# Optimization experiments

Hardware: AMD Instinct MI355X
Metric: run time of the kernel (lower is better)

## Reference

```python
import jax, jax.numpy as jnp
import numpy as np
from jax import lax

K = 5      # reassembly kernel
D = 2      # delta (downsample factor)


def _conv(x, w, b, stride=1, pad=0):
    y = lax.conv_general_dilated(x, w, (stride, stride), [(pad, pad), (pad, pad)],
                                 dimension_numbers=("NCHW", "OIHW", "NCHW"))
    return y + b[None, :, None, None]


def setup_inputs() -> dict:
    key = jax.random.key(0)
    ks = jax.random.split(key, 7)
    inC, outC, Cm = 64, 64, 64
    N, H, W = 2, 256, 256
    return {
        "x": jax.random.normal(ks[0], (N, inC, H, W), jnp.float32),
        "down_w": jax.random.normal(ks[1], (Cm, inC, 1, 1), jnp.float32) * 0.1,
        "down_b": jax.random.normal(ks[2], (Cm,), jnp.float32) * 0.1,
        "enc_w": jax.random.normal(ks[3], (K * K, Cm, 3, 3), jnp.float32) * 0.1,
        "enc_b": jax.random.normal(ks[4], (K * K,), jnp.float32) * 0.1,
        "out_w": jax.random.normal(ks[5], (outC, inC * D * D, 1, 1), jnp.float32) * 0.1,
        "out_b": jax.random.normal(ks[6], (outC,), jnp.float32) * 0.1,
    }


def reference(x, down_w, down_b, enc_w, enc_b, out_w, out_b):
    N, C, H, W = x.shape
    Hd, Wd = H // D, W // D
    p = K // 2

    # kernel prediction branch
    k = _conv(x, down_w, down_b)                       # (N, Cm, H, W)
    k = _conv(k, enc_w, enc_b, stride=D, pad=1)        # (N, K*K, Hd, Wd)
    k = jax.nn.softmax(k, axis=1)
    k = k.transpose(0, 2, 3, 1)                        # (N, Hd, Wd, K*K)

    # overlapping K x K windows at every (h, w): (N, C, H, W, K*K)
    xp = jnp.pad(x, ((0, 0), (0, 0), (p, p), (p, p)))
    patches = jnp.stack([xp[:, :, i:i + H, j:j + W]
                         for i in range(K) for j in range(K)], axis=-1)
    # faithful torch reshape (row-major reinterpretation, NOT space-to-depth)
    patches = patches.reshape(N, C * D * D, Hd, Wd, K * K)
    patches = patches.transpose(0, 2, 3, 1, 4)         # (N, Hd, Wd, C*D*D, K*K)

    out = jnp.einsum("nhwck,nhwk->nhwc", patches, k)   # weighted reassembly
    out = out.transpose(0, 3, 1, 2)                    # (N, C*D*D, Hd, Wd)
    return _conv(out, out_w, out_b)
```

## Files before the change

### kernel.cpp

```cpp
#include <hip/hip_runtime.h>
#include <hip/hip_bf16.h>

using u16 = unsigned short;
typedef __attribute__((ext_vector_type(8))) short bf16x8;
typedef __attribute__((ext_vector_type(4))) float f32x4;

static constexpr int N  = 2;
static constexpr int C  = 64;
static constexpr int H  = 256;
static constexpr int W  = 256;
static constexpr int Hd = 128;
static constexpr int Wd = 128;
static constexpr int KK = 25;
static constexpr int C2 = 256;
static constexpr int OC = 64;
static constexpr int HWP  = H * W;
static constexpr int HDWD = Hd * Wd;

__device__ __forceinline__ float bflo(unsigned u) { return __uint_as_float(u << 16); }
__device__ __forceinline__ float bfhi(unsigned u) { return __uint_as_float(u & 0xffff0000u); }
__device__ __forceinline__ unsigned pack2(float a, float b) {
    __hip_bfloat16 ha = __float2bfloat16(a), hb = __float2bfloat16(b);
    union { __hip_bfloat16 h; u16 u; } ua{ha}, ub{hb};
    return (unsigned)ua.u | ((unsigned)ub.u << 16);
}
__device__ __forceinline__ u16 f2bf(float f) {
    union { __hip_bfloat16 h; u16 u; } v{__float2bfloat16(f)};
    return v.u;
}

__global__ __launch_bounds__(256) void kA_down(const float* __restrict__ x,
                                               const float* __restrict__ w,
                                               const float* __restrict__ b,
                                               u16* __restrict__ k1) {
    __shared__ u16   xt[64][128];
    __shared__ float wt[64][66];
    const int tid = threadIdx.x;
    const int pg0 = blockIdx.x * 128;
    const int n   = pg0 >> 16;
    const int px0 = pg0 & (HWP - 1);

#pragma unroll
    for (int i = 0; i < 16; ++i) {
        int e  = i * 256 + tid;
        int cm = e >> 6, c = e & 63;
        wt[c][cm] = w[e];
    }
    const float* xb = x + (size_t)n * C * HWP + px0;
#pragma unroll
    for (int i = 0; i < 8; ++i) {
        int flat = i * 256 + tid;
        int row  = flat >> 5;
        int col4 = flat & 31;
        float4 v = *(const float4*)(xb + (size_t)row * HWP + col4 * 4);
        uint2 p;
        p.x = pack2(v.x, v.y);
        p.y = pack2(v.z, v.w);
        *(uint2*)&xt[row][col4 * 4] = p;
    }
    __syncthreads();

    const int cg  = tid & 7;
    const int pxg = tid >> 3;
    float acc[8][4];
#pragma unroll
    for (int j = 0; j < 8; ++j) {
        float bj = b[cg * 8 + j];
#pragma unroll
        for (int p = 0; p < 4; ++p) acc[j][p] = bj;
    }
#pragma unroll 8
    for (int c = 0; c < 64; ++c) {
        uint2 xv = *(const uint2*)&xt[c][pxg * 4];
        float xs[4] = {bflo(xv.x), bfhi(xv.x), bflo(xv.y), bfhi(xv.y)};
        float2 w01 = *(const float2*)&wt[c][cg * 8 + 0];
        float2 w23 = *(const float2*)&wt[c][cg * 8 + 2];
        float2 w45 = *(const float2*)&wt[c][cg * 8 + 4];
        float2 w67 = *(const float2*)&wt[c][cg * 8 + 6];
        float wv[8] = {w01.x, w01.y, w23.x, w23.y, w45.x, w45.y, w67.x, w67.y};
#pragma unroll
        for (int j = 0; j < 8; ++j)
#pragma unroll
            for (int p = 0; p < 4; ++p) acc[j][p] = fmaf(wv[j], xs[p], acc[j][p]);
    }
#pragma unroll
    for (int p = 0; p < 4; ++p) {
        uint4 o;
        o.x = pack2(acc[0][p], acc[1][p]);
        o.y = pack2(acc[2][p], acc[3][p]);
        o.z = pack2(acc[4][p], acc[5][p]);
        o.w = pack2(acc[6][p], acc[7][p]);
        *(uint4*)(k1 + ((size_t)pg0 + pxg * 4 + p) * 64 + cg * 8) = o;
    }
}

__global__ __launch_bounds__(256) void kW_pack(const float* __restrict__ ew,
                                               const float* __restrict__ ow,
                                               u16* __restrict__ bfr,
                                               u16* __restrict__ bfr2) {
    int idx = blockIdx.x * 256 + threadIdx.x;
    if (idx < 2304) {
        int l  = idx & 63;
        int ft = idx >> 6;
        int t  = ft & 1, s = ft >> 1;
        int tap = s >> 1, h = s & 1;
        int c = l & 15, q = l >> 4;
        int kk = t * 16 + c;
        u16 o[8];
#pragma unroll
        for (int j = 0; j < 8; ++j) {
            int cm = 32 * h + 8 * q + j;
            float v = (kk < 25) ? ew[(kk * 64 + cm) * 9 + tap] : 0.f;
            o[j] = f2bf(v);
        }
        *(uint4*)(bfr + (size_t)idx * 8) = *(uint4*)o;
    } else if (idx < 4352) {
        int i2 = idx - 2304;
        int l  = i2 & 63;
        int ft = i2 >> 6;
        int nt = ft & 3, s = ft >> 2;
        int c = l & 15, q = l >> 4;
        int co = nt * 16 + c;
        u16 o[8];
#pragma unroll
        for (int j = 0; j < 8; ++j)
            o[j] = f2bf(ow[co * 256 + s * 32 + q * 8 + j]);
        *(uint4*)(bfr2 + (size_t)i2 * 8) = *(uint4*)o;
    }
}

__global__ __launch_bounds__(256) void kB2_enc(const u16* __restrict__ k1,
                                               const u16* __restrict__ bfr,
                                               const float* __restrict__ eb,
                                               float* __restrict__ ksm) {
    __shared__ u16 tile[3 * 130 * 72];
    const int tid = threadIdx.x;
    const int b   = blockIdx.x;
    const int half = b & 1;
    const int hd   = (b >> 1) & 127;
    const int n    = b >> 8;
    const int w0 = half * 64;
    const int xb = 2 * w0 - 1;
    const int y0 = 2 * hd - 1;
    const u16* kb = k1 + (size_t)n * HWP * 64;

    for (int r = 0; r < 13; ++r) {
        int f = r * 256 + tid;
        if (f < 3096) {
            int p  = f >> 3, ch = f & 7;
            int y  = p / 129, xi = p - y * 129;
            int yy = y0 + y, xx = xb + xi;
            uint4 v = make_uint4(0u, 0u, 0u, 0u);
            if (yy >= 0 && xx >= 0 && xx < 256)
                v = *(const uint4*)(kb + ((size_t)(yy * W + xx)) * 64 + ch * 8);
            *(uint4*)&tile[(y * 130 + xi) * 72 + ch * 8] = v;
        }
    }
    __syncthreads();

    const int wv = tid >> 6;
    const int l  = tid & 63;
    const int c  = l & 15;
    const int q  = l >> 4;

    f32x4 acc0 = {0.f, 0.f, 0.f, 0.f};
    f32x4 acc1 = {0.f, 0.f, 0.f, 0.f};
#pragma unroll
    for (int s = 0; s < 18; ++s) {
        const int tap = s >> 1, h = s & 1;
        const int dy = tap / 3, dx = tap - dy * 3;
        const u16* ap = &tile[(dy * 130 + 32 * wv + 2 * c + dx) * 72 + 32 * h + 8 * q];
        bf16x8 a  = *(const bf16x8*)ap;
        bf16x8 b0 = *(const bf16x8*)(bfr + ((size_t)(s * 2 + 0) * 64 + l) * 8);
        bf16x8 b1 = *(const bf16x8*)(bfr + ((size_t)(s * 2 + 1) * 64 + l) * 8);
        acc0 = __builtin_amdgcn_mfma_f32_16x16x32_bf16(a, b0, acc0, 0, 0, 0);
        acc1 = __builtin_amdgcn_mfma_f32_16x16x32_bf16(a, b1, acc1, 0, 0, 0);
    }

    const float e0 = eb[c];
    const float e1 = eb[min(16 + c, 24)];
    const bool c9 = (c < 9);

#pragma unroll
    for (int r = 0; r < 4; ++r) {
        float l0 = acc0[r] + e0;
        float l1 = c9 ? (acc1[r] + e1) : -1e30f;
        float mx = fmaxf(l0, l1);
#pragma unroll
        for (int d = 1; d < 16; d <<= 1) mx = fmaxf(mx, __shfl_xor(mx, d, 64));
        float x0 = __expf(l0 - mx);
        float x1 = c9 ? __expf(l1 - mx) : 0.f;
        float sm = x0 + x1;
#pragma unroll
        for (int d = 1; d < 16; d <<= 1) sm += __shfl_xor(sm, d, 64);
        float inv = 1.f / sm;
        int wd = w0 + 16 * wv + q * 4 + r;
        float* op = ksm + (size_t)n * KK * HDWD + hd * Wd + wd;
        op[(size_t)c * HDWD] = x0 * inv;
        if (c9) op[(size_t)(16 + c) * HDWD] = x1 * inv;
    }
}

__global__ __launch_bounds__(256, 2) void kC8_reassemble(const float* __restrict__ x,
                                                         const float* __restrict__ ksm,
                                                         u16* __restrict__ out2p) {
    __shared__ float xts[4 * 8 * 272];
    const int tid = threadIdx.x;
    const int b   = blockIdx.x;
    const int cc  = b & 31;
    const int hdt = (b >> 5) & 15;
    const int n   = b >> 9;
    const int hd0 = hdt * 8;
    const int t0  = hdt * 4;
    const int hdo = tid >> 5;
    const int wdg = tid & 31;
    const int hd  = hd0 + hdo;
    const int wd0 = wdg * 4;
    const int wb  = ((hdo & 1) << 7) + wd0;
    const int rloc = hdo >> 1;
    const int c0  = cc * 2;

    if (tid < 64) {
        int rr = tid >> 1, side = tid & 1;
        int col = side ? 258 : 0;
        *(float2*)&xts[rr * 272 + col] = make_float2(0.f, 0.f);
    }

    const float* kb = ksm + (size_t)n * KK * HDWD + hd * Wd + wd0;

    int  soff[8];
    bool sval[8];
#pragma unroll
    for (int k = 0; k < 8; ++k) {
        int s     = k * 256 + tid;
        int c4    = s & 63;
        int row   = (s >> 6) & 7;
        int strip = s >> 9;
        int y     = strip * 64 + t0 - 2 + row;
        sval[k]   = (y >= 0) & (y < H);
        int yc    = min(max(y, 0), H - 1);
        soff[k]   = yc * W + c4 * 4;
    }

    unsigned outw[4][4];
    const float4 z4 = make_float4(0.f, 0.f, 0.f, 0.f);

#pragma unroll
    for (int ci = 0; ci < 2; ++ci) {
        __syncthreads();
        const float* base = x + (size_t)(n * C + c0 + ci) * HWP;
#pragma unroll
        for (int k = 0; k < 8; ++k) {
            int s = k * 256 + tid;
            float4 v = sval[k] ? *(const float4*)(base + soff[k]) : z4;
            int widx = (s >> 6) * 272 + 2 + (s & 63) * 4;
            *(float2*)&xts[widx]     = make_float2(v.x, v.y);
            *(float2*)&xts[widx + 2] = make_float2(v.z, v.w);
        }
        __syncthreads();

        float sq[4][4];
#pragma unroll
        for (int q = 0; q < 4; ++q)
#pragma unroll
            for (int r = 0; r < 4; ++r) sq[q][r] = 0.f;

#pragma unroll 1
        for (int ph = 0; ph < 5; ++ph) {
            float4 kwc[5];
#pragma unroll
            for (int j = 0; j < 5; ++j)
                kwc[j] = *(const float4*)(kb + (size_t)(ph * 5 + j) * HDWD);
#pragma unroll
            for (int q = 0; q < 4; ++q) {
                const float* rp = &xts[(q * 8 + rloc + ph) * 272 + wb];
                float4 fa = *(const float4*)(rp);
                float4 fb = *(const float4*)(rp + 4);
                float f[8] = {fa.x, fa.y, fa.z, fa.w, fb.x, fb.y, fb.z, fb.w};
#pragma unroll
                for (int j = 0; j < 5; ++j) {
                    const float4 kv = kwc[j];
                    sq[q][0] = fmaf(f[j + 0], kv.x, sq[q][0]);
                    sq[q][1] = fmaf(f[j + 1], kv.y, sq[q][1]);
                    sq[q][2] = fmaf(f[j + 2], kv.z, sq[q][2]);
                    sq[q][3] = fmaf(f[j + 3], kv.w, sq[q][3]);
                }
            }
        }
#pragma unroll
        for (int r = 0; r < 4; ++r) {
            outw[r][ci * 2 + 0] = pack2(sq[0][r], sq[1][r]);
            outw[r][ci * 2 + 1] = pack2(sq[2][r], sq[3][r]);
        }
    }

    u16* dst = out2p + ((size_t)(n * 32 + cc) * HDWD + hd * Wd + wd0) * 8;
#pragma unroll
    for (int r = 0; r < 4; ++r) {
        uint4 wa = make_uint4(outw[r][0], outw[r][1], outw[r][2], outw[r][3]);
        *(uint4*)(dst + (size_t)r * 8) = wa;
    }
}

__global__ __launch_bounds__(256) void kD3_out(const u16* __restrict__ out2p,
                                               const u16* __restrict__ bfr2,
                                               const float* __restrict__ ob,
                                               float* __restrict__ out) {
    const int tid = threadIdx.x;
    const int b   = blockIdx.x;
    const int px0g = b * 64;
    const int n    = px0g >> 14;
    const int px0  = px0g & (HDWD - 1);
    const int nt = tid >> 6;
    const int l  = tid & 63;
    const int c  = l & 15;
    const int q  = l >> 4;

    const u16* An = out2p + (size_t)n * 32 * HDWD * 8;

    f32x4 acc[4] = {{0.f,0.f,0.f,0.f},{0.f,0.f,0.f,0.f},
                    {0.f,0.f,0.f,0.f},{0.f,0.f,0.f,0.f}};
#pragma unroll
    for (int s = 0; s < 8; ++s) {
        bf16x8 bf = *(const bf16x8*)(bfr2 + ((size_t)(s * 4 + nt) * 64 + l) * 8);
#pragma unroll
        for (int mt = 0; mt < 4; ++mt) {
            const u16* ap = An + ((size_t)(4 * s + q) * HDWD + px0 + mt * 16 + c) * 8;
            bf16x8 a = *(const bf16x8*)ap;
            acc[mt] = __builtin_amdgcn_mfma_f32_16x16x32_bf16(a, bf, acc[mt], 0, 0, 0);
        }
    }
    const int co = nt * 16 + c;
    const float bias = ob[co];
    float* ob_ = out + (size_t)(n * OC + co) * HDWD + px0;
#pragma unroll
    for (int mt = 0; mt < 4; ++mt)
#pragma unroll
        for (int r = 0; r < 4; ++r)
            ob_[mt * 16 + q * 4 + r] = acc[mt][r] + bias;
}

extern "C" void kernel_launch(void* const* d_in, const int* in_sizes, int n_in,
                              void* d_out, int out_size, void* d_ws, size_t ws_size,
                              hipStream_t stream) {
    const float* x  = (const float*)d_in[0];
    const float* dw = (const float*)d_in[1];
    const float* db = (const float*)d_in[2];
    const float* ew = (const float*)d_in[3];
    const float* eb = (const float*)d_in[4];
    const float* ow = (const float*)d_in[5];
    const float* ob = (const float*)d_in[6];
    float* out = (float*)d_out;

    char* ws = (char*)d_ws;
    u16*   k1    = (u16*)ws;
    float* ksm   = (float*)(ws + 16777216);
    u16*   out2p = (u16*)(ws + 16777216 + 3276800);
    u16*   bfr   = out2p;
    u16*   bfr2  = (u16*)(ws + 16777216 + 3276800 + 16777216);

    kW_pack <<<dim3(18),   dim3(256), 0, stream>>>(ew, ow, bfr, bfr2);
    kA_down <<<dim3(1024), dim3(256), 0, stream>>>(x, dw, db, k1);
    kB2_enc <<<dim3(512),  dim3(256), 0, stream>>>(k1, bfr, eb, ksm);
    kC8_reassemble<<<dim3(1024), dim3(256), 0, stream>>>(x, ksm, out2p);
    kD3_out <<<dim3(512),  dim3(256), 0, stream>>>(out2p, bfr2, ob, out);
}
```

Baseline: 150.1 us.

## Fuse weight packing into down conv and software-pipeline reassembly loads

The separate weight-packing kernel is folded into the first 18 blocks of the down-projection kernel, removing one launch. The reassembly kernel is unrolled over its two channels. It double-buffers the per-phase softmax kernel-weight loads and prefetches half of the second channel's x tile into registers while the first channel computes. This hides global load latency at the cost of higher register pressure, which may hurt occupancy under the two-blocks-per-SM launch bound.

```diff
diff --git a/kernel.cpp b/kernel.cpp
--- a/kernel.cpp
+++ b/kernel.cpp
@@ -32,7 +32,11 @@
 __global__ __launch_bounds__(256) void kA_down(const float* __restrict__ x,
                                                const float* __restrict__ w,
                                                const float* __restrict__ b,
-                                               u16* __restrict__ k1) {
+                                               u16* __restrict__ k1,
+                                               const float* __restrict__ ew,
+                                               const float* __restrict__ ow,
+                                               u16* __restrict__ bfr,
+                                               u16* __restrict__ bfr2) {
     __shared__ u16   xt[64][128];
     __shared__ float wt[64][66];
     const int tid = threadIdx.x;
@@ -92,40 +96,37 @@
         o.w = pack2(acc[6][p], acc[7][p]);
         *(uint4*)(k1 + ((size_t)pg0 + pxg * 4 + p) * 64 + cg * 8) = o;
     }
-}
-
-__global__ __launch_bounds__(256) void kW_pack(const float* __restrict__ ew,
-                                               const float* __restrict__ ow,
-                                               u16* __restrict__ bfr,
-                                               u16* __restrict__ bfr2) {
-    int idx = blockIdx.x * 256 + threadIdx.x;
-    if (idx < 2304) {
-        int l  = idx & 63;
-        int ft = idx >> 6;
-        int t  = ft & 1, s = ft >> 1;
-        int tap = s >> 1, h = s & 1;
-        int c = l & 15, q = l >> 4;
-        int kk = t * 16 + c;
-        u16 o[8];
-#pragma unroll
-        for (int j = 0; j < 8; ++j) {
-            int cm = 32 * h + 8 * q + j;
-            float v = (kk < 25) ? ew[(kk * 64 + cm) * 9 + tap] : 0.f;
-            o[j] = f2bf(v);
+
+    if (blockIdx.x < 18) {
+        int idx = blockIdx.x * 256 + tid;
+        if (idx < 2304) {
+            int l  = idx & 63;
+            int ft = idx >> 6;
+            int t  = ft & 1, s = ft >> 1;
+            int tap = s >> 1, h = s & 1;
+            int c = l & 15, q = l >> 4;
+            int kk = t * 16 + c;
+            u16 o[8];
+#pragma unroll
+            for (int j = 0; j < 8; ++j) {
+                int cm = 32 * h + 8 * q + j;
+                float v = (kk < 25) ? ew[(kk * 64 + cm) * 9 + tap] : 0.f;
+                o[j] = f2bf(v);
+            }
+            *(uint4*)(bfr + (size_t)idx * 8) = *(uint4*)o;
+        } else if (idx < 4352) {
+            int i2 = idx - 2304;
+            int l  = i2 & 63;
+            int ft = i2 >> 6;
+            int nt = ft & 3, s = ft >> 2;
+            int c = l & 15, q = l >> 4;
+            int co = nt * 16 + c;
+            u16 o[8];
+#pragma unroll
+            for (int j = 0; j < 8; ++j)
+                o[j] = f2bf(ow[co * 256 + s * 32 + q * 8 + j]);
+            *(uint4*)(bfr2 + (size_t)i2 * 8) = *(uint4*)o;
         }
-        *(uint4*)(bfr + (size_t)idx * 8) = *(uint4*)o;
-    } else if (idx < 4352) {
-        int i2 = idx - 2304;
-        int l  = i2 & 63;
-        int ft = i2 >> 6;
-        int nt = ft & 3, s = ft >> 2;
-        int c = l & 15, q = l >> 4;
-        int co = nt * 16 + c;
-        u16 o[8];
-#pragma unroll
-        for (int j = 0; j < 8; ++j)
-            o[j] = f2bf(ow[co * 256 + s * 32 + q * 8 + j]);
-        *(uint4*)(bfr2 + (size_t)i2 * 8) = *(uint4*)o;
     }
 }
 
@@ -201,7 +202,7 @@
     }
 }
 
-__global__ __launch_bounds__(256, 2) void kC8_reassemble(const float* __restrict__ x,
+__global__ __launch_bounds__(256, 2) void kC9_reassemble(const float* __restrict__ x,
                                                          const float* __restrict__ ksm,
                                                          u16* __restrict__ out2p) {
     __shared__ float xts[4 * 8 * 272];
@@ -245,53 +246,103 @@
     unsigned outw[4][4];
     const float4 z4 = make_float4(0.f, 0.f, 0.f, 0.f);
 
-#pragma unroll
-    for (int ci = 0; ci < 2; ++ci) {
-        __syncthreads();
-        const float* base = x + (size_t)(n * C + c0 + ci) * HWP;
-#pragma unroll
-        for (int k = 0; k < 8; ++k) {
-            int s = k * 256 + tid;
-            float4 v = sval[k] ? *(const float4*)(base + soff[k]) : z4;
-            int widx = (s >> 6) * 272 + 2 + (s & 63) * 4;
-            *(float2*)&xts[widx]     = make_float2(v.x, v.y);
-            *(float2*)&xts[widx + 2] = make_float2(v.z, v.w);
-        }
-        __syncthreads();
-
-        float sq[4][4];
-#pragma unroll
-        for (int q = 0; q < 4; ++q)
-#pragma unroll
-            for (int r = 0; r < 4; ++r) sq[q][r] = 0.f;
-
-#pragma unroll 1
-        for (int ph = 0; ph < 5; ++ph) {
-            float4 kwc[5];
-#pragma unroll
-            for (int j = 0; j < 5; ++j)
-                kwc[j] = *(const float4*)(kb + (size_t)(ph * 5 + j) * HDWD);
-#pragma unroll
-            for (int q = 0; q < 4; ++q) {
-                const float* rp = &xts[(q * 8 + rloc + ph) * 272 + wb];
-                float4 fa = *(const float4*)(rp);
-                float4 fb = *(const float4*)(rp + 4);
-                float f[8] = {fa.x, fa.y, fa.z, fa.w, fb.x, fb.y, fb.z, fb.w};
-#pragma unroll
-                for (int j = 0; j < 5; ++j) {
-                    const float4 kv = kwc[j];
-                    sq[q][0] = fmaf(f[j + 0], kv.x, sq[q][0]);
-                    sq[q][1] = fmaf(f[j + 1], kv.y, sq[q][1]);
-                    sq[q][2] = fmaf(f[j + 2], kv.z, sq[q][2]);
-                    sq[q][3] = fmaf(f[j + 3], kv.w, sq[q][3]);
-                }
+    const float* base0 = x + (size_t)(n * C + c0) * HWP;
+    const float* base1 = base0 + HWP;
+
+    auto widx = [&](int s) { return (s >> 6) * 272 + 2 + (s & 63) * 4; };
+
+    auto loadK = [&](float4 kw[5], int ph) {
+#pragma unroll
+        for (int j = 0; j < 5; ++j)
+            kw[j] = *(const float4*)(kb + (size_t)(ph * 5 + j) * HDWD);
+    };
+    float sq[4][4];
+    auto doPhase = [&](const float4 kw[5], int ph) {
+#pragma unroll
+        for (int q = 0; q < 4; ++q) {
+            const float* rp = &xts[(q * 8 + rloc + ph) * 272 + wb];
+            float4 fa = *(const float4*)(rp);
+            float4 fb = *(const float4*)(rp + 4);
+            float f[8] = {fa.x, fa.y, fa.z, fa.w, fb.x, fb.y, fb.z, fb.w};
+#pragma unroll
+            for (int j = 0; j < 5; ++j) {
+                const float4 kv = kw[j];
+                sq[q][0] = fmaf(f[j + 0], kv.x, sq[q][0]);
+                sq[q][1] = fmaf(f[j + 1], kv.y, sq[q][1]);
+                sq[q][2] = fmaf(f[j + 2], kv.z, sq[q][2]);
+                sq[q][3] = fmaf(f[j + 3], kv.w, sq[q][3]);
             }
         }
-#pragma unroll
-        for (int r = 0; r < 4; ++r) {
-            outw[r][ci * 2 + 0] = pack2(sq[0][r], sq[1][r]);
-            outw[r][ci * 2 + 1] = pack2(sq[2][r], sq[3][r]);
-        }
+    };
+    auto resetSq = [&]() {
+#pragma unroll
+        for (int q = 0; q < 4; ++q)
+#pragma unroll
+            for (int r = 0; r < 4; ++r) sq[q][r] = 0.f;
+    };
+
+    __syncthreads();
+#pragma unroll
+    for (int k = 0; k < 8; ++k) {
+        int s = k * 256 + tid;
+        float4 v = sval[k] ? *(const float4*)(base0 + soff[k]) : z4;
+        int wi = widx(s);
+        *(float2*)&xts[wi]     = make_float2(v.x, v.y);
+        *(float2*)&xts[wi + 2] = make_float2(v.z, v.w);
+    }
+    __syncthreads();
+
+    float4 kwA[5], kwB[5];
+    loadK(kwA, 0);
+
+    float4 xp[4];
+#pragma unroll
+    for (int k = 0; k < 4; ++k)
+        xp[k] = sval[k] ? *(const float4*)(base1 + soff[k]) : z4;
+
+    resetSq();
+    loadK(kwB, 1); doPhase(kwA, 0);
+    loadK(kwA, 2); doPhase(kwB, 1);
+    loadK(kwB, 3); doPhase(kwA, 2);
+    loadK(kwA, 4); doPhase(kwB, 3);
+    doPhase(kwA, 4);
+
+#pragma unroll
+    for (int r = 0; r < 4; ++r) {
+        outw[r][0] = pack2(sq[0][r], sq[1][r]);
+        outw[r][1] = pack2(sq[2][r], sq[3][r]);
+    }
+
+    __syncthreads();
+#pragma unroll
+    for (int k = 0; k < 4; ++k) {
+        int s = k * 256 + tid;
+        int wi = widx(s);
+        *(float2*)&xts[wi]     = make_float2(xp[k].x, xp[k].y);
+        *(float2*)&xts[wi + 2] = make_float2(xp[k].z, xp[k].w);
+    }
+#pragma unroll
+    for (int k = 4; k < 8; ++k) {
+        int s = k * 256 + tid;
+        float4 v = sval[k] ? *(const float4*)(base1 + soff[k]) : z4;
+        int wi = widx(s);
+        *(float2*)&xts[wi]     = make_float2(v.x, v.y);
+        *(float2*)&xts[wi + 2] = make_float2(v.z, v.w);
+    }
+    __syncthreads();
+
+    loadK(kwA, 0);
+    resetSq();
+    loadK(kwB, 1); doPhase(kwA, 0);
+    loadK(kwA, 2); doPhase(kwB, 1);
+    loadK(kwB, 3); doPhase(kwA, 2);
+    loadK(kwA, 4); doPhase(kwB, 3);
+    doPhase(kwA, 4);
+
+#pragma unroll
+    for (int r = 0; r < 4; ++r) {
+        outw[r][2] = pack2(sq[0][r], sq[1][r]);
+        outw[r][3] = pack2(sq[2][r], sq[3][r]);
     }
 
     u16* dst = out2p + ((size_t)(n * 32 + cc) * HDWD + hd * Wd + wd0) * 8;
@@ -359,9 +410,8 @@
     u16*   bfr   = out2p;
     u16*   bfr2  = (u16*)(ws + 16777216 + 3276800 + 16777216);
 
-    kW_pack <<<dim3(18),   dim3(256), 0, stream>>>(ew, ow, bfr, bfr2);
-    kA_down <<<dim3(1024), dim3(256), 0, stream>>>(x, dw, db, k1);
+    kA_down <<<dim3(1024), dim3(256), 0, stream>>>(x, dw, db, k1, ew, ow, bfr, bfr2);
     kB2_enc <<<dim3(512),  dim3(256), 0, stream>>>(k1, bfr, eb, ksm);
-    kC8_reassemble<<<dim3(1024), dim3(256), 0, stream>>>(x, ksm, out2p);
+    kC9_reassemble<<<dim3(1024), dim3(256), 0, stream>>>(x, ksm, out2p);
     kD3_out <<<dim3(512),  dim3(256), 0, stream>>>(out2p, bfr2, ob, out);
 }
```

New measurement: 189.5 us. +26.2%, slower.
